# Performance work log

Hardware: AMD Instinct MI355X
Metric: run time of the kernel (lower is better)

The kernel has to match this reference:

```python
import jax, jax.numpy as jnp
import numpy as np

N_HEAD = 16
D_HEAD = 64
D_HIDN = 1024
B, S = 2, 2048
MASK_FILL = -1e9


def setup_inputs() -> dict:
    key = jax.random.key(0)
    ks = jax.random.split(key, 8)
    scale = 1.0 / np.sqrt(D_HIDN)
    return {
        "Q": jax.random.normal(ks[0], (B, S, D_HIDN), dtype=jnp.float32),
        "K": jax.random.normal(ks[1], (B, S, D_HIDN), dtype=jnp.float32),
        "V": jax.random.normal(ks[2], (B, S, D_HIDN), dtype=jnp.float32),
        "attn_mask": jnp.zeros((B, S, S), dtype=jnp.bool_),
        "Wq": jax.random.normal(ks[3], (D_HIDN, N_HEAD * D_HEAD), dtype=jnp.float32) * scale,
        "bq": jnp.zeros((N_HEAD * D_HEAD,), dtype=jnp.float32),
        "Wk": jax.random.normal(ks[4], (D_HIDN, N_HEAD * D_HEAD), dtype=jnp.float32) * scale,
        "bk": jnp.zeros((N_HEAD * D_HEAD,), dtype=jnp.float32),
        "Wv": jax.random.normal(ks[5], (D_HIDN, N_HEAD * D_HEAD), dtype=jnp.float32) * scale,
        "bv": jnp.zeros((N_HEAD * D_HEAD,), dtype=jnp.float32),
        "Wo": jax.random.normal(ks[6], (N_HEAD * D_HEAD, D_HIDN), dtype=jnp.float32) * scale,
        "bo": jnp.zeros((D_HIDN,), dtype=jnp.float32),
    }


def reference(Q, K, V, attn_mask, Wq, bq, Wk, bk, Wv, bv, Wo, bo):
    b, s, _ = Q.shape
    # projections -> [B, H, S, d_head]
    def split_heads(x):
        return x.reshape(b, -1, N_HEAD, D_HEAD).transpose(0, 2, 1, 3)
    q = split_heads(Q @ Wq + bq)
    k = split_heads(K @ Wk + bk)
    v = split_heads(V @ Wv + bv)
    # scaled dot-product attention with masked_fill(-1e9)
    scores = jnp.einsum("bhqd,bhkd->bhqk", q, k) / jnp.sqrt(jnp.float32(D_HEAD))
    scores = jnp.where(attn_mask[:, None, :, :], MASK_FILL, scores)
    attn_prob = jax.nn.softmax(scores, axis=-1)  # [B,H,S,S]
    context = jnp.einsum("bhqk,bhkd->bhqd", attn_prob, v)
    context = context.transpose(0, 2, 1, 3).reshape(b, s, N_HEAD * D_HEAD)
    output = context @ Wo + bo  # dropout is identity at eval
    return output, attn_prob
```

## Files before the change

### kernel.cpp

```cpp
#include <hip/hip_runtime.h>

typedef _Float16 f16;
typedef _Float16 f16x8 __attribute__((ext_vector_type(8)));
typedef _Float16 f16x4v __attribute__((ext_vector_type(4)));
typedef float f32x4 __attribute__((ext_vector_type(4)));

#define B_   2
#define S_   2048
#define H_   16
#define DH   64
#define DM   1024
#define BS_  (B_ * S_)

#if __has_builtin(__builtin_amdgcn_exp2f)
#define EXP2(x) __builtin_amdgcn_exp2f(x)
#else
#define EXP2(x) exp2f(x)
#endif

#define SCHED_FENCE() __builtin_amdgcn_sched_barrier(0)

__device__ __forceinline__ void gload16(const void* g, void* l) {
  __builtin_amdgcn_global_load_lds((const __attribute__((address_space(1))) unsigned int*)g,
                                   (__attribute__((address_space(3))) unsigned int*)l, 16, 0, 0);
}

__global__ __launch_bounds__(256) void prep(const float* __restrict__ Q, const float* __restrict__ K,
                                            const float* __restrict__ V,
                                            f16* __restrict__ Xq, f16* __restrict__ Xk, f16* __restrict__ Xv,
                                            const float* __restrict__ w0, const float* __restrict__ w1,
                                            const float* __restrict__ w2, const float* __restrict__ w3,
                                            f16* __restrict__ t0, f16* __restrict__ t1,
                                            f16* __restrict__ t2, f16* __restrict__ t3) {
  int bid = blockIdx.x;
  int tid = threadIdx.x;
  if (bid < 6144) {
    int t = bid >> 11;
    const float* in = t == 0 ? Q : (t == 1 ? K : V);
    f16* out = t == 0 ? Xq : (t == 1 ? Xk : Xv);
    int i = ((bid & 2047) * 256 + tid) * 8;
    float4 x = *(const float4*)(in + i);
    float4 y = *(const float4*)(in + i + 4);
    f16x8 o;
    o[0] = (f16)x.x; o[1] = (f16)x.y; o[2] = (f16)x.z; o[3] = (f16)x.w;
    o[4] = (f16)y.x; o[5] = (f16)y.y; o[6] = (f16)y.z; o[7] = (f16)y.w;
    *(f16x8*)(out + i) = o;
  } else {
    __shared__ float t[64][65];
    int w = bid - 6144;
    int z = w >> 8, rr = w & 255;
    const float* wsrc = z == 0 ? w0 : (z == 1 ? w1 : (z == 2 ? w2 : w3));
    f16* wt = z == 0 ? t0 : (z == 1 ? t1 : (z == 2 ? t2 : t3));
    int r0 = (rr >> 4) * 64, c0 = (rr & 15) * 64;
    int tr = tid >> 2, seg = tid & 3;
#pragma unroll
    for (int jj = 0; jj < 4; ++jj) {
      float4 v = *(const float4*)(wsrc + (size_t)(r0 + tr) * DM + c0 + seg * 16 + jj * 4);
      t[tr][seg * 16 + jj * 4 + 0] = v.x;
      t[tr][seg * 16 + jj * 4 + 1] = v.y;
      t[tr][seg * 16 + jj * 4 + 2] = v.z;
      t[tr][seg * 16 + jj * 4 + 3] = v.w;
    }
    __syncthreads();
#pragma unroll
    for (int jj = 0; jj < 2; ++jj) {
      f16x8 o;
#pragma unroll
      for (int e = 0; e < 8; ++e) o[e] = (f16)t[seg * 16 + jj * 8 + e][tr];
      *(f16x8*)(wt + (size_t)(c0 + tr) * DM + r0 + seg * 16 + jj * 8) = o;
    }
  }
}

__device__ __forceinline__ void gemm_core(const f16* __restrict__ A,
                                          const f16* __restrict__ Bt,
                                          int m0, int n0,
                                          char (&As)[2][16384], char (&Bs)[2][16384],
                                          f32x4 (&acc)[4][2]) {
  const int tid = threadIdx.x;
  const int lane = tid & 63, wid = tid >> 6;
  const int wr = wid >> 2, wc = wid & 3;
  const int l15 = lane & 15, l4 = lane >> 4;
#pragma unroll
  for (int mi = 0; mi < 4; ++mi)
#pragma unroll
    for (int ni = 0; ni < 2; ++ni) { acc[mi][ni][0]=0.f; acc[mi][ni][1]=0.f; acc[mi][ni][2]=0.f; acc[mi][ni][3]=0.f; }

  auto stage = [&](int buf, int kt) {
#pragma unroll
    for (int j = 0; j < 2; ++j) {
      int L = j * 512 + tid;
      int row = L >> 3, seg = L & 7;
      int so = (seg ^ (row & 7)) << 4;
      gload16((const char*)A + ((size_t)(m0 + row) * DM + kt) * 2 + so,
              As[buf] + j * 8192 + wid * 1024);
      gload16((const char*)Bt + ((size_t)(n0 + row) * DM + kt) * 2 + so,
              Bs[buf] + j * 8192 + wid * 1024);
    }
  };

  stage(0, 0);
  __syncthreads();
  for (int t = 0; t < 16; ++t) {
    int cur = t & 1;
    if (t < 15) stage(cur ^ 1, (t + 1) * 64);
#pragma unroll
    for (int kk = 0; kk < 2; ++kk) {
      f16x8 af[4], bf[2];
#pragma unroll
      for (int mi = 0; mi < 4; ++mi) {
        int row = wr * 64 + mi * 16 + l15;
        af[mi] = *(const f16x8*)(As[cur] + row * 128 + ((kk * 64 + l4 * 16) ^ ((row & 7) << 4)));
      }
#pragma unroll
      for (int ni = 0; ni < 2; ++ni) {
        int row = wc * 32 + ni * 16 + l15;
        bf[ni] = *(const f16x8*)(Bs[cur] + row * 128 + ((kk * 64 + l4 * 16) ^ ((row & 7) << 4)));
      }
#pragma unroll
      for (int mi = 0; mi < 4; ++mi)
#pragma unroll
        for (int ni = 0; ni < 2; ++ni)
          acc[mi][ni] = __builtin_amdgcn_mfma_f32_16x16x32_f16(af[mi], bf[ni], acc[mi][ni], 0, 0, 0);
    }
    __syncthreads();
  }
}

struct GemmPtrs { const f16* A; const f16* Bt; const float* bias; f16* outh; };

__global__ __launch_bounds__(512, 4) void gemm_proj(GemmPtrs p0, GemmPtrs p1, GemmPtrs p2,
                                                    f16* __restrict__ vout) {
  __shared__ __attribute__((aligned(16))) char As[2][16384];
  __shared__ __attribute__((aligned(16))) char Bs[2][16384];
  int lin = (blockIdx.z * 8 + blockIdx.y) * 32 + blockIdx.x;
  int swz = (lin & 7) * 96 + (lin >> 3);
  int z = swz >> 8, r = swz & 255;
  int m0 = (r >> 3) * 128, n0 = (r & 7) * 128;
  GemmPtrs g = z == 0 ? p0 : (z == 1 ? p1 : p2);

  f32x4 acc[4][2];
  gemm_core(g.A, g.Bt, m0, n0, As, Bs, acc);

  const int tid = threadIdx.x;
  const int lane = tid & 63, wid = tid >> 6;
  const int wr = wid >> 2, wc = wid & 3;
  const int l15 = lane & 15, l4 = lane >> 4;

  if (z != 2) {
#pragma unroll
    for (int mi = 0; mi < 4; ++mi)
#pragma unroll
      for (int ni = 0; ni < 2; ++ni) {
        int gcol = n0 + wc * 32 + ni * 16 + l15;
        float bv = g.bias[gcol];
#pragma unroll
        for (int rr = 0; rr < 4; ++rr) {
          int grow = m0 + wr * 64 + mi * 16 + l4 * 4 + rr;
          int b = grow >> 11, s = grow & 2047, h = gcol >> 6, d = gcol & 63;
          g.outh[(size_t)((b * H_ + h) * S_ + s) * DH + d] = (f16)(acc[mi][ni][rr] + bv);
        }
      }
  } else {
    f16* T2 = (f16*)&As[0][0];
    int b = m0 >> 11, s0 = m0 & 2047;
#pragma unroll
    for (int hh = 0; hh < 2; ++hh) {
      if ((wc >> 1) == hh) {
        int dl = (wc & 1) * 32;
#pragma unroll
        for (int mi = 0; mi < 4; ++mi)
#pragma unroll
          for (int ni = 0; ni < 2; ++ni) {
            int d = dl + ni * 16 + l15;
            int sl = wr * 64 + mi * 16 + l4 * 4;
            float bv = g.bias[n0 + hh * 64 + d];
            f16x4v pv;
            pv[0] = (f16)(acc[mi][ni][0] + bv);
            pv[1] = (f16)(acc[mi][ni][1] + bv);
            pv[2] = (f16)(acc[mi][ni][2] + bv);
            pv[3] = (f16)(acc[mi][ni][3] + bv);
            *(f16x4v*)(T2 + d * 136 + sl) = pv;
          }
      }
      __syncthreads();
      {
        int d = tid >> 3, sq = tid & 7;
        int head = (n0 >> 6) + hh;
        const f16* src = T2 + d * 136 + sq * 16;
        f16* dst = vout + ((size_t)((b * H_ + head) * DH + d)) * S_ + s0 + sq * 16;
        *(f16x8*)(dst)     = *(const f16x8*)(src);
        *(f16x8*)(dst + 8) = *(const f16x8*)(src + 8);
      }
      if (hh == 0) __syncthreads();
    }
  }
}

__global__ __launch_bounds__(512, 2) void gemm_out(const f16* __restrict__ A,
                                                   const f16* __restrict__ Bt,
                                                   const float* __restrict__ bias,
                                                   float* __restrict__ outf) {
  __shared__ __attribute__((aligned(16))) char As[2][16384];
  __shared__ __attribute__((aligned(16))) char Bs[2][16384];
  int lin = blockIdx.y * 32 + blockIdx.x;
  int swz = (lin & 7) * 32 + (lin >> 3);
  int m0 = (swz >> 3) * 128, n0 = (swz & 7) * 128;

  f32x4 acc[4][2];
  gemm_core(A, Bt, m0, n0, As, Bs, acc);

  const int tid = threadIdx.x;
  const int lane = tid & 63, wid = tid >> 6;
  const int wr = wid >> 2, wc = wid & 3;
  const int l15 = lane & 15, l4 = lane >> 4;
#pragma unroll
  for (int mi = 0; mi < 4; ++mi)
#pragma unroll
    for (int ni = 0; ni < 2; ++ni) {
      int gcol = n0 + wc * 32 + ni * 16 + l15;
      float bv = bias[gcol];
#pragma unroll
      for (int rr = 0; rr < 4; ++rr) {
        int grow = m0 + wr * 64 + mi * 16 + l4 * 4 + rr;
        outf[(size_t)grow * DM + gcol] = acc[mi][ni][rr] + bv;
      }
    }
}

__global__ __launch_bounds__(512, 4) void attn_kernel(const f16* __restrict__ q,
                                                      const f16* __restrict__ k,
                                                      const f16* __restrict__ vt,
                                                      const unsigned char* __restrict__ mask,
                                                      float* __restrict__ pout,
                                                      f16* __restrict__ ctxh) {
  __shared__ __attribute__((aligned(16))) char KV[4][8192];
  __shared__ __attribute__((aligned(16))) float P32[8][16][68];
  const int tid = threadIdx.x;
  const int lane = tid & 63, wid = tid >> 6;
  const int l15 = lane & 15, l4 = lane >> 4;

  int lin = blockIdx.y * 16 + blockIdx.x;
  int swz = (lin & 7) * 64 + (lin >> 3);
  const int bx = swz & 15, bh = swz >> 4;
  const int b = bh >> 4, h = bh & 15;
  const int q0w = bx * 128 + wid * 16;

  const f16* qb = q + (size_t)bh * S_ * DH;
  const char* kbc = (const char*)(k + (size_t)bh * S_ * DH);
  const char* vtbc = (const char*)(vt + (size_t)bh * DH * S_);
  const unsigned char* mb = mask + (size_t)b * S_ * S_;
  float* pb = pout + (size_t)bh * S_ * S_;

  const int srow = tid >> 3, sseg = tid & 7;
  const int soff = (sseg ^ (srow & 7)) << 4;

  auto stageK = [&](int buf, int t) {
    gload16(kbc + (size_t)(t * 64 + srow) * 128 + soff, KV[buf] + wid * 1024);
  };
  auto stageV = [&](int buf, int t) {
    gload16(vtbc + (size_t)srow * (S_ * 2) + (size_t)(t * 64) * 2 + soff, KV[buf] + wid * 1024);
  };

  unsigned mmask = 0;
  {
    const unsigned char* mrow = mb + (size_t)(q0w + (lane >> 2)) * S_ + (lane & 3) * 16;
    unsigned acc_or = 0;
#pragma unroll
    for (int tt = 0; tt < 4; ++tt) {
      uint4 mu[8];
#pragma unroll
      for (int u = 0; u < 8; ++u) mu[u] = *(const uint4*)(mrow + (tt * 8 + u) * 64);
#pragma unroll
      for (int u = 0; u < 8; ++u) acc_or |= mu[u].x | mu[u].y | mu[u].z | mu[u].w;
    }
    if (__any(acc_or != 0)) {
      for (int t = 0; t < 32; ++t) {
        uint4 mu = *(const uint4*)(mrow + t * 64);
        if (__any((mu.x | mu.y | mu.z | mu.w) != 0)) mmask |= 1u << t;
      }
    }
  }

  const f16 qs = (f16)0.18033688f;
  f16x8 aq[2];
#pragma unroll
  for (int hh = 0; hh < 2; ++hh) {
    f16x8 v = *(const f16x8*)(qb + (size_t)(q0w + l15) * DH + hh * 32 + l4 * 8);
#pragma unroll
    for (int j = 0; j < 8; ++j) v[j] = v[j] * qs;
    aq[hh] = v;
  }
  SCHED_FENCE();

  float sm[4] = {0.f, 0.f, 0.f, 0.f};

  stageK(0, 0);
  stageK(1, 1);
  for (int p = 0; p < 16; ++p) {
    asm volatile("s_waitcnt vmcnt(0)" ::: "memory");
    __builtin_amdgcn_s_barrier();
    SCHED_FENCE();
    if (p < 15) { stageK((2 * p + 2) & 3, 2 * p + 2); stageK((2 * p + 3) & 3, 2 * p + 3); }
    SCHED_FENCE();
#pragma unroll
    for (int u = 0; u < 2; ++u) {
      const int t = 2 * p + u;
      const char* Kb = KV[t & 3];
      const int kt = t * 64;
      const int anym = (mmask >> t) & 1;
#pragma unroll
      for (int f = 0; f < 4; ++f) {
        int krow = f * 16 + l15;
        f16x8 bk0 = *(const f16x8*)(Kb + krow * 128 + ((l4 * 16) ^ ((krow & 7) << 4)));
        f16x8 bk1 = *(const f16x8*)(Kb + krow * 128 + ((64 + l4 * 16) ^ ((krow & 7) << 4)));
        f32x4 s; s[0]=0.f; s[1]=0.f; s[2]=0.f; s[3]=0.f;
        __builtin_amdgcn_s_setprio(1);
        s = __builtin_amdgcn_mfma_f32_16x16x32_f16(aq[0], bk0, s, 0, 0, 0);
        s = __builtin_amdgcn_mfma_f32_16x16x32_f16(aq[1], bk1, s, 0, 0, 0);
        __builtin_amdgcn_s_setprio(0);
#pragma unroll
        for (int rr = 0; rr < 4; ++rr) {
          float sv = s[rr];
          if (anym) sv = mb[(size_t)(q0w + l4 * 4 + rr) * S_ + kt + f * 16 + l15] ? -1e9f : sv;
          sm[rr] += EXP2(sv);
        }
      }
    }
  }
#pragma unroll
  for (int d = 1; d < 16; d <<= 1)
#pragma unroll
    for (int rr = 0; rr < 4; ++rr) sm[rr] += __shfl_xor(sm[rr], d);
  float inv[4];
#pragma unroll
  for (int rr = 0; rr < 4; ++rr) inv[rr] = 1.0f / sm[rr];

  f32x4 ctx[4];
#pragma unroll
  for (int dc = 0; dc < 4; ++dc) { ctx[dc][0]=0.f; ctx[dc][1]=0.f; ctx[dc][2]=0.f; ctx[dc][3]=0.f; }

  __builtin_amdgcn_s_barrier();
  stageK(0, 0);
  stageV(2, 0);
  __syncthreads();
  for (int t = 0; t < 32; ++t) {
    const int cur = t & 1;
    const int kt = t * 64;
    if (t < 31) { stageK(cur ^ 1, t + 1); stageV(2 + (cur ^ 1), t + 1); }
    SCHED_FENCE();
    const int anym = (mmask >> t) & 1;

#pragma unroll
    for (int f = 0; f < 4; ++f) {
      int krow = f * 16 + l15;
      f16x8 bk0 = *(const f16x8*)(KV[cur] + krow * 128 + ((l4 * 16) ^ ((krow & 7) << 4)));
      f16x8 bk1 = *(const f16x8*)(KV[cur] + krow * 128 + ((64 + l4 * 16) ^ ((krow & 7) << 4)));
      f32x4 s; s[0]=0.f; s[1]=0.f; s[2]=0.f; s[3]=0.f;
      __builtin_amdgcn_s_setprio(1);
      s = __builtin_amdgcn_mfma_f32_16x16x32_f16(aq[0], bk0, s, 0, 0, 0);
      s = __builtin_amdgcn_mfma_f32_16x16x32_f16(aq[1], bk1, s, 0, 0, 0);
      __builtin_amdgcn_s_setprio(0);
#pragma unroll
      for (int rr = 0; rr < 4; ++rr) {
        float sv = s[rr];
        if (anym) sv = mb[(size_t)(q0w + l4 * 4 + rr) * S_ + kt + f * 16 + l15] ? -1e9f : sv;
        float p = EXP2(sv) * inv[rr];
        P32[wid][l4 * 4 + rr][f * 16 + l15] = p;
      }
    }
#pragma unroll
    for (int j = 0; j < 4; ++j) {
      int row = j * 4 + l4;
      f32x4 v = *(const f32x4*)&P32[wid][row][l15 * 4];
      __builtin_nontemporal_store(v, (f32x4*)(pb + (size_t)(q0w + row) * S_ + kt + l15 * 4));
    }
#pragma unroll
    for (int kk = 0; kk < 2; ++kk) {
      f32x4 x = *(const f32x4*)&P32[wid][l15][kk * 32 + l4 * 8];
      f32x4 y = *(const f32x4*)&P32[wid][l15][kk * 32 + l4 * 8 + 4];
      f16x8 pa;
      pa[0] = (f16)x[0]; pa[1] = (f16)x[1]; pa[2] = (f16)x[2]; pa[3] = (f16)x[3];
      pa[4] = (f16)y[0]; pa[5] = (f16)y[1]; pa[6] = (f16)y[2]; pa[7] = (f16)y[3];
      f16x8 bv0, bv1, bv2, bv3;
      {
        int vr0 = 0 * 16 + l15, vr1 = 1 * 16 + l15, vr2 = 2 * 16 + l15, vr3 = 3 * 16 + l15;
        bv0 = *(const f16x8*)(KV[2 + cur] + vr0 * 128 + ((kk * 64 + l4 * 16) ^ ((vr0 & 7) << 4)));
        bv1 = *(const f16x8*)(KV[2 + cur] + vr1 * 128 + ((kk * 64 + l4 * 16) ^ ((vr1 & 7) << 4)));
        bv2 = *(const f16x8*)(KV[2 + cur] + vr2 * 128 + ((kk * 64 + l4 * 16) ^ ((vr2 & 7) << 4)));
        bv3 = *(const f16x8*)(KV[2 + cur] + vr3 * 128 + ((kk * 64 + l4 * 16) ^ ((vr3 & 7) << 4)));
      }
      __builtin_amdgcn_s_setprio(1);
      ctx[0] = __builtin_amdgcn_mfma_f32_16x16x32_f16(pa, bv0, ctx[0], 0, 0, 0);
      ctx[1] = __builtin_amdgcn_mfma_f32_16x16x32_f16(pa, bv1, ctx[1], 0, 0, 0);
      ctx[2] = __builtin_amdgcn_mfma_f32_16x16x32_f16(pa, bv2, ctx[2], 0, 0, 0);
      ctx[3] = __builtin_amdgcn_mfma_f32_16x16x32_f16(pa, bv3, ctx[3], 0, 0, 0);
      __builtin_amdgcn_s_setprio(0);
    }

    if (t < 31) {
      asm volatile("s_waitcnt vmcnt(4)" ::: "memory");
      __builtin_amdgcn_s_barrier();
      SCHED_FENCE();
    }
  }

#pragma unroll
  for (int dc = 0; dc < 4; ++dc)
#pragma unroll
    for (int rr = 0; rr < 4; ++rr)
      ctxh[(size_t)(b * S_ + q0w + l4 * 4 + rr) * DM + h * DH + dc * 16 + l15] = (f16)ctx[dc][rr];
}

extern "C" void kernel_launch(void* const* d_in, const int* in_sizes, int n_in,
                              void* d_out, int out_size, void* d_ws, size_t ws_size,
                              hipStream_t stream) {
  (void)in_sizes; (void)n_in; (void)out_size; (void)ws_size;
  const float* Q  = (const float*)d_in[0];
  const float* K  = (const float*)d_in[1];
  const float* V  = (const float*)d_in[2];
  const unsigned char* mask = (const unsigned char*)d_in[3];
  const float* Wq = (const float*)d_in[4];
  const float* bq = (const float*)d_in[5];
  const float* Wk = (const float*)d_in[6];
  const float* bk = (const float*)d_in[7];
  const float* Wv = (const float*)d_in[8];
  const float* bv = (const float*)d_in[9];
  const float* Wo = (const float*)d_in[10];
  const float* bo = (const float*)d_in[11];

  f16* ws = (f16*)d_ws;
  f16* Xq  = ws;
  f16* Xk  = Xq + 4194304;
  f16* Xv  = Xk + 4194304;
  f16* Wqt = Xv + 4194304;
  f16* Wkt = Wqt + 1048576;
  f16* Wvt = Wkt + 1048576;
  f16* Wot = Wvt + 1048576;
  f16* qh  = Wot + 1048576;
  f16* kh  = qh + 4194304;
  f16* vth = kh + 4194304;
  f16* ctx = Xq;

  float* out0 = (float*)d_out;
  float* pout = out0 + (size_t)BS_ * DM;

  prep<<<dim3(7168), dim3(256), 0, stream>>>(Q, K, V, Xq, Xk, Xv,
                                             Wq, Wk, Wv, Wo, Wqt, Wkt, Wvt, Wot);

  GemmPtrs pq{Xq, Wqt, bq, qh};
  GemmPtrs pk{Xk, Wkt, bk, kh};
  GemmPtrs pv{Xv, Wvt, bv, nullptr};
  gemm_proj<<<dim3(32, 8, 3), dim3(512), 0, stream>>>(pq, pk, pv, vth);

  attn_kernel<<<dim3(16, 32), dim3(512), 0, stream>>>(qh, kh, vth, mask, pout, ctx);

  gemm_out<<<dim3(32, 8), dim3(512), 0, stream>>>(ctx, Wot, bo, out0);
}
```

Measured before the change: 224.2 us.

## Precompute mask tile bitmap in prep, deepen K pipeline, coalesce context stores

Mask-tile occupancy bits are now computed once per (batch, query-tile) in extra prep blocks and written to a small table. Previously every attention block (16 heads each) rescanned the mask rows itself. The first-pass K loop now stages one tile per iteration with three in flight and partial vmcnt waits, replacing two tiles staged behind a full vmcnt(0) drain. The context output is transposed through LDS so it is written as wider contiguous stores. The cost is extra prep work and a workspace table, plus a barrier on every tile instead of every pair of tiles.

Result: slower. 231.4 us (+3.2%).

```diff
diff --git a/kernel.cpp b/kernel.cpp
--- a/kernel.cpp
+++ b/kernel.cpp
@@ -31,7 +31,9 @@
                                             const float* __restrict__ w0, const float* __restrict__ w1,
                                             const float* __restrict__ w2, const float* __restrict__ w3,
                                             f16* __restrict__ t0, f16* __restrict__ t1,
-                                            f16* __restrict__ t2, f16* __restrict__ t3) {
+                                            f16* __restrict__ t2, f16* __restrict__ t3,
+                                            const unsigned char* __restrict__ mask,
+                                            unsigned* __restrict__ mtab) {
   int bid = blockIdx.x;
   int tid = threadIdx.x;
   if (bid < 6144) {
@@ -45,7 +47,7 @@
     o[0] = (f16)x.x; o[1] = (f16)x.y; o[2] = (f16)x.z; o[3] = (f16)x.w;
     o[4] = (f16)y.x; o[5] = (f16)y.y; o[6] = (f16)y.z; o[7] = (f16)y.w;
     *(f16x8*)(out + i) = o;
-  } else {
+  } else if (bid < 7168) {
     __shared__ float t[64][65];
     int w = bid - 6144;
     int z = w >> 8, rr = w & 255;
@@ -69,6 +71,28 @@
       for (int e = 0; e < 8; ++e) o[e] = (f16)t[seg * 16 + jj * 8 + e][tr];
       *(f16x8*)(wt + (size_t)(c0 + tr) * DM + r0 + seg * 16 + jj * 8) = o;
     }
+  } else {
+    __shared__ unsigned mbits;
+    if (tid == 0) mbits = 0;
+    __syncthreads();
+    int mb_id = bid - 7168;
+    int b = mb_id >> 4, qt = mb_id & 15;
+    int row = qt * 128 + (tid >> 1), halfsel = tid & 1;
+    const unsigned char* mrow = mask + (size_t)b * S_ * S_ + (size_t)row * S_ + halfsel * 1024;
+    unsigned bits = 0;
+#pragma unroll
+    for (int c = 0; c < 16; ++c) {
+      uint4 a0 = *(const uint4*)(mrow + c * 64);
+      uint4 a1 = *(const uint4*)(mrow + c * 64 + 16);
+      uint4 a2 = *(const uint4*)(mrow + c * 64 + 32);
+      uint4 a3 = *(const uint4*)(mrow + c * 64 + 48);
+      unsigned z = (a0.x|a0.y|a0.z|a0.w) | (a1.x|a1.y|a1.z|a1.w) |
+                   (a2.x|a2.y|a2.z|a2.w) | (a3.x|a3.y|a3.z|a3.w);
+      bits |= (z != 0 ? 1u : 0u) << (halfsel * 16 + c);
+    }
+    if (bits) atomicOr(&mbits, bits);
+    __syncthreads();
+    if (tid == 0) mtab[mb_id] = mbits;
   }
 }
 
@@ -232,6 +256,7 @@
                                                       const f16* __restrict__ k,
                                                       const f16* __restrict__ vt,
                                                       const unsigned char* __restrict__ mask,
+                                                      const unsigned* __restrict__ mtab,
                                                       float* __restrict__ pout,
                                                       f16* __restrict__ ctxh) {
   __shared__ __attribute__((aligned(16))) char KV[4][8192];
@@ -262,25 +287,7 @@
     gload16(vtbc + (size_t)srow * (S_ * 2) + (size_t)(t * 64) * 2 + soff, KV[buf] + wid * 1024);
   };
 
-  unsigned mmask = 0;
-  {
-    const unsigned char* mrow = mb + (size_t)(q0w + (lane >> 2)) * S_ + (lane & 3) * 16;
-    unsigned acc_or = 0;
-#pragma unroll
-    for (int tt = 0; tt < 4; ++tt) {
-      uint4 mu[8];
-#pragma unroll
-      for (int u = 0; u < 8; ++u) mu[u] = *(const uint4*)(mrow + (tt * 8 + u) * 64);
-#pragma unroll
-      for (int u = 0; u < 8; ++u) acc_or |= mu[u].x | mu[u].y | mu[u].z | mu[u].w;
-    }
-    if (__any(acc_or != 0)) {
-      for (int t = 0; t < 32; ++t) {
-        uint4 mu = *(const uint4*)(mrow + t * 64);
-        if (__any((mu.x | mu.y | mu.z | mu.w) != 0)) mmask |= 1u << t;
-      }
-    }
-  }
+  const unsigned mmask = mtab[b * 16 + bx];
 
   const f16 qs = (f16)0.18033688f;
   f16x8 aq[2];
@@ -297,34 +304,34 @@
 
   stageK(0, 0);
   stageK(1, 1);
-  for (int p = 0; p < 16; ++p) {
-    asm volatile("s_waitcnt vmcnt(0)" ::: "memory");
+  stageK(2, 2);
+  for (int t = 0; t < 32; ++t) {
+    SCHED_FENCE();
+    if (t < 30)       asm volatile("s_waitcnt vmcnt(2)" ::: "memory");
+    else if (t == 30) asm volatile("s_waitcnt vmcnt(1)" ::: "memory");
+    else              asm volatile("s_waitcnt vmcnt(0)" ::: "memory");
     __builtin_amdgcn_s_barrier();
     SCHED_FENCE();
-    if (p < 15) { stageK((2 * p + 2) & 3, 2 * p + 2); stageK((2 * p + 3) & 3, 2 * p + 3); }
-    SCHED_FENCE();
-#pragma unroll
-    for (int u = 0; u < 2; ++u) {
-      const int t = 2 * p + u;
-      const char* Kb = KV[t & 3];
-      const int kt = t * 64;
-      const int anym = (mmask >> t) & 1;
-#pragma unroll
-      for (int f = 0; f < 4; ++f) {
-        int krow = f * 16 + l15;
-        f16x8 bk0 = *(const f16x8*)(Kb + krow * 128 + ((l4 * 16) ^ ((krow & 7) << 4)));
-        f16x8 bk1 = *(const f16x8*)(Kb + krow * 128 + ((64 + l4 * 16) ^ ((krow & 7) << 4)));
-        f32x4 s; s[0]=0.f; s[1]=0.f; s[2]=0.f; s[3]=0.f;
-        __builtin_amdgcn_s_setprio(1);
-        s = __builtin_amdgcn_mfma_f32_16x16x32_f16(aq[0], bk0, s, 0, 0, 0);
-        s = __builtin_amdgcn_mfma_f32_16x16x32_f16(aq[1], bk1, s, 0, 0, 0);
-        __builtin_amdgcn_s_setprio(0);
-#pragma unroll
-        for (int rr = 0; rr < 4; ++rr) {
-          float sv = s[rr];
-          if (anym) sv = mb[(size_t)(q0w + l4 * 4 + rr) * S_ + kt + f * 16 + l15] ? -1e9f : sv;
-          sm[rr] += EXP2(sv);
-        }
+    if (t < 29) stageK((t + 3) & 3, t + 3);
+
+    const char* Kb = KV[t & 3];
+    const int kt = t * 64;
+    const int anym = (mmask >> t) & 1;
+#pragma unroll
+    for (int f = 0; f < 4; ++f) {
+      int krow = f * 16 + l15;
+      f16x8 bk0 = *(const f16x8*)(Kb + krow * 128 + ((l4 * 16) ^ ((krow & 7) << 4)));
+      f16x8 bk1 = *(const f16x8*)(Kb + krow * 128 + ((64 + l4 * 16) ^ ((krow & 7) << 4)));
+      f32x4 s; s[0]=0.f; s[1]=0.f; s[2]=0.f; s[3]=0.f;
+      __builtin_amdgcn_s_setprio(1);
+      s = __builtin_amdgcn_mfma_f32_16x16x32_f16(aq[0], bk0, s, 0, 0, 0);
+      s = __builtin_amdgcn_mfma_f32_16x16x32_f16(aq[1], bk1, s, 0, 0, 0);
+      __builtin_amdgcn_s_setprio(0);
+#pragma unroll
+      for (int rr = 0; rr < 4; ++rr) {
+        float sv = s[rr];
+        if (anym) sv = mb[(size_t)(q0w + l4 * 4 + rr) * S_ + kt + f * 16 + l15] ? -1e9f : sv;
+        sm[rr] += EXP2(sv);
       }
     }
   }
@@ -405,11 +412,20 @@
     }
   }
 
-#pragma unroll
-  for (int dc = 0; dc < 4; ++dc)
-#pragma unroll
-    for (int rr = 0; rr < 4; ++rr)
-      ctxh[(size_t)(b * S_ + q0w + l4 * 4 + rr) * DM + h * DH + dc * 16 + l15] = (f16)ctx[dc][rr];
+  {
+    f16* cst = (f16*)&P32[wid][0][0];
+#pragma unroll
+    for (int dc = 0; dc < 4; ++dc)
+#pragma unroll
+      for (int rr = 0; rr < 4; ++rr)
+        cst[(l4 * 4 + rr) * 72 + dc * 16 + l15] = (f16)ctx[dc][rr];
+#pragma unroll
+    for (int j = 0; j < 4; ++j) {
+      int row = j * 4 + l4;
+      f16x4v v = *(const f16x4v*)(cst + row * 72 + l15 * 4);
+      *(f16x4v*)(ctxh + (size_t)(b * S_ + q0w + row) * DM + h * DH + l15 * 4) = v;
+    }
+  }
 }
 
 extern "C" void kernel_launch(void* const* d_in, const int* in_sizes, int n_in,
@@ -440,20 +456,22 @@
   f16* qh  = Wot + 1048576;
   f16* kh  = qh + 4194304;
   f16* vth = kh + 4194304;
+  unsigned* mtab = (unsigned*)(vth + 4194304);
   f16* ctx = Xq;
 
   float* out0 = (float*)d_out;
   float* pout = out0 + (size_t)BS_ * DM;
 
-  prep<<<dim3(7168), dim3(256), 0, stream>>>(Q, K, V, Xq, Xk, Xv,
-                                             Wq, Wk, Wv, Wo, Wqt, Wkt, Wvt, Wot);
+  prep<<<dim3(7200), dim3(256), 0, stream>>>(Q, K, V, Xq, Xk, Xv,
+                                             Wq, Wk, Wv, Wo, Wqt, Wkt, Wvt, Wot,
+                                             mask, mtab);
 
   GemmPtrs pq{Xq, Wqt, bq, qh};
   GemmPtrs pk{Xk, Wkt, bk, kh};
   GemmPtrs pv{Xv, Wvt, bv, nullptr};
   gemm_proj<<<dim3(32, 8, 3), dim3(512), 0, stream>>>(pq, pk, pv, vth);
 
-  attn_kernel<<<dim3(16, 32), dim3(512), 0, stream>>>(qh, kh, vth, mask, pout, ctx);
+  attn_kernel<<<dim3(16, 32), dim3(512), 0, stream>>>(qh, kh, vth, mask, mtab, pout, ctx);
 
   gemm_out<<<dim3(32, 8), dim3(512), 0, stream>>>(ctx, Wot, bo, out0);
 }
```
